# Performance work log

Hardware: AMD Instinct MI355X
Metric: run time of the kernel (lower is better)

## Reference

```python
import jax, jax.numpy as jnp
import numpy as np

N, M, C, IN, OUT = 65536, 512, 512, 256, 256
EPS = 1e-8


def setup_inputs() -> dict:
    key = jax.random.key(0)
    ks = jax.random.split(key, 12)
    d = {}
    d["x"] = jax.random.normal(ks[0], (1, IN), jnp.float32)
    d["memory"] = jax.random.normal(ks[1], (1, N, M), jnp.float32) * 0.05
    d["prev_read"] = jax.random.normal(ks[2], (1, M), jnp.float32) * 0.05
    d["h"] = jnp.ones((1, C), jnp.float32)
    d["c"] = jnp.ones((1, C), jnp.float32)
    d["read_state"] = jnp.zeros((1, N), jnp.float32)
    d["write_state"] = jnp.zeros((1, N), jnp.float32)
    d["W_ih"] = jax.random.normal(ks[3], (4 * C, IN + M), jnp.float32) * 0.02
    d["b_ih"] = jax.random.normal(ks[4], (4 * C,), jnp.float32) * 0.01
    d["W_hh"] = jax.random.normal(ks[5], (4 * C, C), jnp.float32) * 0.02
    d["b_hh"] = jax.random.normal(ks[6], (4 * C,), jnp.float32) * 0.01
    d["W_read"] = jax.random.normal(ks[7], (M + 6, C), jnp.float32) * 0.02
    d["b_read"] = jnp.zeros((M + 6,), jnp.float32)
    d["W_write"] = jax.random.normal(ks[8], (3 * M + 6, C), jnp.float32) * 0.02
    d["b_write"] = jnp.zeros((3 * M + 6,), jnp.float32)
    d["W_out"] = jax.random.normal(ks[9], (OUT, C + M), jnp.float32) * 0.02
    d["b_out"] = jnp.zeros((OUT,), jnp.float32)
    return d


def _address(head_out, w_prev, memory):
    # head_out: [B, M+6(+...)]; returns sharpened addressing weights [B, N]
    key_v = head_out[:, :M]
    beta = jax.nn.softplus(head_out[:, M:M + 1])          # [B,1]
    g = jax.nn.sigmoid(head_out[:, M + 1:M + 2])          # [B,1]
    shift = jax.nn.softmax(head_out[:, M + 2:M + 5], axis=1)  # [B,3]
    gamma = 1.0 + jax.nn.softplus(head_out[:, M + 5:M + 6])   # [B,1]
    # content addressing: cosine similarity over memory rows
    a = memory + EPS                                      # [B,N,M]
    b = key_v[:, None, :] + EPS                           # [B,1,M]
    dot = jnp.sum(a * b, axis=-1)                         # [B,N]
    na = jnp.maximum(jnp.sqrt(jnp.sum(a * a, axis=-1)), EPS)
    nb = jnp.maximum(jnp.sqrt(jnp.sum(b * b, axis=-1)), EPS)
    cos = dot / (na * nb)
    w_context = jax.nn.softmax(beta * cos, axis=1)        # [B,N]
    # NOTE: original code swaps args -> g gates the PREVIOUS weights
    w_interp = g * w_prev + (1.0 - g) * w_context
    # circular shift via 3-tap correlation (conv1d with circular pad)
    w_pad = jnp.concatenate([w_interp[:, -1:], w_interp, w_interp[:, :1]], axis=1)
    w_shift = (w_pad[:, :-2] * shift[:, 0:1]
               + w_pad[:, 1:-1] * shift[:, 1:2]
               + w_pad[:, 2:] * shift[:, 2:3])
    power = w_shift ** gamma
    return power / (jnp.sum(power, axis=1, keepdims=True) + EPS)


def reference(x, memory, prev_read, h, c, read_state, write_state,
              W_ih, b_ih, W_hh, b_hh, W_read, b_read, W_write, b_write,
              W_out, b_out):
    # LSTMCell controller (torch gate order: i, f, g, o)
    inp = jnp.concatenate([x, prev_read], axis=1)                   # [B, IN+M]
    gates = inp @ W_ih.T + b_ih + h @ W_hh.T + b_hh                 # [B, 4C]
    i_g, f_g, g_g, o_g = jnp.split(gates, 4, axis=1)
    c_new = jax.nn.sigmoid(f_g) * c + jax.nn.sigmoid(i_g) * jnp.tanh(g_g)
    h_new = jax.nn.sigmoid(o_g) * jnp.tanh(c_new)

    # read head
    r_out = h_new @ W_read.T + b_read
    w_r = _address(r_out, read_state, memory)                       # [B,N]
    # faithful to torch.matmul([B,N],[B,N,M]).sum(1): sums weights over batch
    read = jnp.einsum('n,bnm->bm', jnp.sum(w_r, axis=0), memory)    # [B,M]

    # write head
    w_out_head = h_new @ W_write.T + b_write
    w_w = _address(w_out_head, write_state, memory)                 # [B,N]
    erase = jax.nn.sigmoid(w_out_head[:, M + 6:2 * M + 6])          # [B,M]
    add = w_out_head[:, 2 * M + 6:3 * M + 6]                        # [B,M]
    memory_new = memory * (1.0 - w_w[:, :, None] * erase[:, None, :]) \
                 + w_w[:, :, None] * add[:, None, :]                # [B,N,M]

    out = jax.nn.sigmoid(jnp.concatenate([h_new, read], axis=1) @ W_out.T + b_out)
    del memory_new  # state update; torch forward returns only the output
    return out
```

## Files before the change

kernel.cpp:

```cpp
#include <hip/hip_runtime.h>
#include <math.h>

#define EPS 1e-8f
#define NN 65536
#define MAGIC 1.0f

#define WS_GATES 0
#define WS_HNEW  2048
#define WS_ROUT  2560
#define WS_PMAX  3104
#define WS_PEXP  5152
#define WS_S     7200
#define WS_PSUM  72736
#define WS_PART  72992
#define WS_FLAGG 204064
#define WS_FLAGP 204192
#define WS_BF    262144

__device__ __forceinline__ float wave_sum(float v) {
    for (int o = 32; o > 0; o >>= 1) v += __shfl_xor(v, o);
    return v;
}
__device__ __forceinline__ float sigm(float x) { return 1.f / (1.f + expf(-x)); }
__device__ __forceinline__ float softplusf_(float x) {
    return x > 20.f ? x : log1pf(expf(x));
}
__device__ __forceinline__ float dot4(float4 a, float4 b) {
    return a.x * b.x + a.y * b.y + a.z * b.z + a.w * b.w;
}
__device__ __forceinline__ float4 ld4(const float* p) { return *(const float4*)p; }

__device__ __forceinline__ float ald(const float* p) {
    return __hip_atomic_load(p, __ATOMIC_RELAXED, __HIP_MEMORY_SCOPE_AGENT);
}
__device__ __forceinline__ float ald_acq(const float* p) {
    return __hip_atomic_load(p, __ATOMIC_ACQUIRE, __HIP_MEMORY_SCOPE_AGENT);
}
__device__ __forceinline__ void ast(float* p, float v) {
    __hip_atomic_store(p, v, __ATOMIC_RELAXED, __HIP_MEMORY_SCOPE_AGENT);
}
__device__ __forceinline__ void ast_rel(float* p, float v) {
    __hip_atomic_store(p, v, __ATOMIC_RELEASE, __HIP_MEMORY_SCOPE_AGENT);
}
__device__ __forceinline__ float2 ald2(const float* p) {
    unsigned long long u = __hip_atomic_load((const unsigned long long*)p,
        __ATOMIC_RELAXED, __HIP_MEMORY_SCOPE_AGENT);
    float2 r; __builtin_memcpy(&r, &u, 8); return r;
}
__device__ __forceinline__ void ast2(float* p, float2 v) {
    unsigned long long u; __builtin_memcpy(&u, &v, 8);
    __hip_atomic_store((unsigned long long*)p, u,
        __ATOMIC_RELAXED, __HIP_MEMORY_SCOPE_AGENT);
}

__device__ __forceinline__ unsigned bf2(float a, float b) {
    unsigned ua = __float_as_uint(a), ub = __float_as_uint(b);
    unsigned ra = (ua + 0x7FFFu + ((ua >> 16) & 1u)) >> 16;
    unsigned rb = (ub + 0x7FFFu + ((ub >> 16) & 1u)) >> 16;
    return ra | (rb << 16);
}

__global__ __launch_bounds__(256) void k_front(const float* __restrict__ x,
                                               const float* __restrict__ pr,
                                               const float* __restrict__ h,
                                               const float* __restrict__ c,
                                               const float* __restrict__ W_ih,
                                               const float* __restrict__ b_ih,
                                               const float* __restrict__ W_hh,
                                               const float* __restrict__ b_hh,
                                               const float* __restrict__ W_read,
                                               const float* __restrict__ b_read,
                                               float* __restrict__ ws) {
    const int b = blockIdx.x, t = threadIdx.x;
    const int lane = t & 63, wv = t >> 6;
    __shared__ float sh[512];

    if (b < 128) {
        #pragma unroll
        for (int i = 0; i < 4; ++i) {
            const int row = b * 16 + wv * 4 + i;
            const float* wi = W_ih + (size_t)row * 768;
            const float* wh = W_hh + (size_t)row * 512;
            float acc = dot4(ld4(wi + lane * 4), ld4(x + lane * 4))
                      + dot4(ld4(wi + 256 + lane * 4), ld4(pr + lane * 4))
                      + dot4(ld4(wi + 512 + lane * 4), ld4(pr + 256 + lane * 4))
                      + dot4(ld4(wh + lane * 4), ld4(h + lane * 4))
                      + dot4(ld4(wh + 256 + lane * 4), ld4(h + 256 + lane * 4));
            acc = wave_sum(acc);
            if (lane == 0) ast(ws + WS_GATES + row, acc + b_ih[row] + b_hh[row]);
        }
        __syncthreads();
        if (t == 0) ast_rel(ws + WS_FLAGG + b, MAGIC);
    }

    if (wv == 0) {
        int cap = 0;
        for (;;) {
            float v0 = ald_acq(ws + WS_FLAGG + lane);
            float v1 = ald_acq(ws + WS_FLAGG + 64 + lane);
            if (__all(v0 == MAGIC && v1 == MAGIC)) break;
            __builtin_amdgcn_s_sleep(1);
            if (++cap > (1 << 20)) break;
        }
    }
    __syncthreads();

    for (int j = t; j < 512; j += 256) {
        float ig = ald(ws + WS_GATES + j);
        float fg = ald(ws + WS_GATES + 512 + j);
        float gg = ald(ws + WS_GATES + 1024 + j);
        float og = ald(ws + WS_GATES + 1536 + j);
        float cn = sigm(fg) * c[j] + sigm(ig) * tanhf(gg);
        float hn = sigm(og) * tanhf(cn);
        sh[j] = hn;
        if (b == 0) ws[WS_HNEW + j] = hn;
    }
    __syncthreads();
    const int o = b * 4 + wv;
    if (o < 518) {
        const float* wr = W_read + (size_t)o * 512;
        float acc = dot4(ld4(wr + lane * 4), ld4(sh + lane * 4))
                  + dot4(ld4(wr + 256 + lane * 4), ld4(sh + 256 + lane * 4));
        acc = wave_sum(acc);
        if (lane == 0) ws[WS_ROUT + o] = acc + b_read[o];
    }
}

__global__ __launch_bounds__(256, 4) void k_cos(const float* __restrict__ mem,
                                                float* __restrict__ ws) {
    const int t = threadIdx.x, lane = t & 63, wv = t >> 6;
    const int gw = blockIdx.x * 4 + wv;
    const float* key = ws + WS_ROUT;
    unsigned short* wsb = (unsigned short*)(ws + WS_BF);
    float4 ka = ld4(key + lane * 4);
    float4 kb = ld4(key + 256 + lane * 4);
    ka.x += EPS; ka.y += EPS; ka.z += EPS; ka.w += EPS;
    kb.x += EPS; kb.y += EPS; kb.z += EPS; kb.w += EPS;
    const float nb = fmaxf(__builtin_amdgcn_sqrtf(
                        wave_sum(dot4(ka, ka) + dot4(kb, kb))), EPS);
    const float beta = softplusf_(key[512]);
    float* sp = ws + WS_S;

    float d[8], q[8];
    #pragma unroll
    for (int grp = 0; grp < 2; ++grp) {
        float4 va[4], vb[4];
        #pragma unroll
        for (int i = 0; i < 4; ++i) {
            const size_t n = (size_t)gw + (grp * 4 + i) * 8192;
            va[i] = ld4(mem + n * 512 + lane * 4);
            vb[i] = ld4(mem + n * 512 + 256 + lane * 4);
        }
        #pragma unroll
        for (int i = 0; i < 4; ++i) {
            const size_t n = (size_t)gw + (grp * 4 + i) * 8192;
            uint2 p0 = make_uint2(bf2(va[i].x, va[i].y), bf2(va[i].z, va[i].w));
            uint2 p1 = make_uint2(bf2(vb[i].x, vb[i].y), bf2(vb[i].z, vb[i].w));
            *(uint2*)(wsb + n * 512 + lane * 4) = p0;
            *(uint2*)(wsb + n * 512 + 256 + lane * 4) = p1;
            va[i].x += EPS; va[i].y += EPS; va[i].z += EPS; va[i].w += EPS;
            vb[i].x += EPS; vb[i].y += EPS; vb[i].z += EPS; vb[i].w += EPS;
            d[grp * 4 + i] = dot4(va[i], ka) + dot4(vb[i], kb);
            q[grp * 4 + i] = dot4(va[i], va[i]) + dot4(vb[i], vb[i]);
        }
    }
    #pragma unroll
    for (int o = 32; o > 0; o >>= 1) {
        #pragma unroll
        for (int i = 0; i < 8; ++i) {
            d[i] += __shfl_xor(d[i], o);
            q[i] += __shfl_xor(q[i], o);
        }
    }
    float sv[8];
    #pragma unroll
    for (int i = 0; i < 8; ++i) {
        float na = fmaxf(__builtin_amdgcn_sqrtf(q[i]), EPS);
        sv[i] = beta * d[i] * __builtin_amdgcn_rcpf(na * nb);
    }
    {
        float mysv = sv[0];
        #pragma unroll
        for (int i = 1; i < 8; ++i) if (lane == i) mysv = sv[i];
        if (lane < 8) sp[gw + lane * 8192] = mysv;
    }
    float m01 = fmaxf(sv[0], sv[1]), m23 = fmaxf(sv[2], sv[3]);
    float m45 = fmaxf(sv[4], sv[5]), m67 = fmaxf(sv[6], sv[7]);
    float m = fmaxf(fmaxf(m01, m23), fmaxf(m45, m67));
    float e = 0.f;
    #pragma unroll
    for (int i = 0; i < 8; ++i) e += __expf(sv[i] - m);

    __shared__ float sm[4], se[4];
    if (lane == 0) { sm[wv] = m; se[wv] = e; }
    __syncthreads();
    if (t == 0) {
        float M = fmaxf(fmaxf(sm[0], sm[1]), fmaxf(sm[2], sm[3]));
        float E = se[0] * __expf(sm[0] - M) + se[1] * __expf(sm[1] - M) +
                  se[2] * __expf(sm[2] - M) + se[3] * __expf(sm[3] - M);
        ws[WS_PMAX + blockIdx.x] = M;
        ws[WS_PEXP + blockIdx.x] = E;
    }
}

__global__ __launch_bounds__(512) void k_readout(const float* __restrict__ rs,
                                                 const float* __restrict__ W_out,
                                                 const float* __restrict__ b_out,
                                                 float* __restrict__ ws,
                                                 float* __restrict__ out) {
    const int b = blockIdx.x, t = threadIdx.x;
    const int lane = t & 63, wv = t >> 6;
    __shared__ float s_m[8], s_e[8];
    __shared__ float wi_l[258];
    __shared__ float pl[256];
    __shared__ float s_ps[4];
    __shared__ float sacc[8][512];
    __shared__ float rd[512];
    __shared__ float s_z[8];

    float m = -1e30f, e = 0.f;
    for (int i = t; i < 2048; i += 512) {
        float bm = ws[WS_PMAX + i], be = ws[WS_PEXP + i];
        float nm = fmaxf(m, bm);
        e = e * expf(m - nm) + be * expf(bm - nm);
        m = nm;
    }
    for (int o = 32; o > 0; o >>= 1) {
        float om = __shfl_xor(m, o), oe = __shfl_xor(e, o);
        float nm = fmaxf(m, om);
        e = e * expf(m - nm) + oe * expf(om - nm);
        m = nm;
    }
    if (lane == 0) { s_m[wv] = m; s_e[wv] = e; }
    __syncthreads();
    float mx = s_m[0];
    for (int i = 1; i < 8; ++i) mx = fmaxf(mx, s_m[i]);
    float Z = 0.f;
    for (int i = 0; i < 8; ++i) Z += s_e[i] * expf(s_m[i] - mx);
    const float invZ = 1.f / Z;
    const float g = sigm(ws[WS_ROUT + 513]);
    float a3 = ws[WS_ROUT + 514], b3 = ws[WS_ROUT + 515], c3 = ws[WS_ROUT + 516];
    float mm = fmaxf(a3, fmaxf(b3, c3));
    float ea = expf(a3 - mm), eb = expf(b3 - mm), ec = expf(c3 - mm);
    float ss = ea + eb + ec;
    const float s0 = ea / ss, s1 = eb / ss, s2 = ec / ss;
    const float gamma = 1.f + softplusf_(ws[WS_ROUT + 517]);

    const int start = b * 256;
    const float* sp = ws + WS_S;
    if (t < 258) {
        int idx = (start - 1 + t) & (NN - 1);
        wi_l[t] = g * rs[idx] + (1.f - g) * expf(sp[idx] - mx) * invZ;
    }
    __syncthreads();
    float ps = 0.f;
    if (t < 256) {
        float wsh = wi_l[t] * s0 + wi_l[t + 1] * s1 + wi_l[t + 2] * s2;
        float pv = powf(wsh, gamma);
        pl[t] = pv;
        ps = pv;
    }
    ps = wave_sum(ps);
    if (t < 256 && lane == 0) s_ps[wv] = ps;
    __syncthreads();
    if (t == 0) ast(ws + WS_PSUM + b, s_ps[0] + s_ps[1] + s_ps[2] + s_ps[3]);

    {
        const unsigned short* wsb = (const unsigned short*)(ws + WS_BF);
        float a0 = 0.f, a1 = 0.f, a2 = 0.f, a3f = 0.f,
              a4 = 0.f, a5 = 0.f, a6 = 0.f, a7 = 0.f;
        #pragma unroll 4
        for (int r = wv; r < 256; r += 8) {
            float w = pl[r];
            uint4 qv = *(const uint4*)(wsb + (size_t)(start + r) * 512 + lane * 8);
            a0 += w * __uint_as_float(qv.x << 16);
            a1 += w * __uint_as_float(qv.x & 0xFFFF0000u);
            a2 += w * __uint_as_float(qv.y << 16);
            a3f += w * __uint_as_float(qv.y & 0xFFFF0000u);
            a4 += w * __uint_as_float(qv.z << 16);
            a5 += w * __uint_as_float(qv.z & 0xFFFF0000u);
            a6 += w * __uint_as_float(qv.w << 16);
            a7 += w * __uint_as_float(qv.w & 0xFFFF0000u);
        }
        float* sw = &sacc[wv][lane * 8];
        sw[0] = a0; sw[1] = a1; sw[2] = a2; sw[3] = a3f;
        sw[4] = a4; sw[5] = a5; sw[6] = a6; sw[7] = a7;
    }
    __syncthreads();
    if (t < 256) {
        const int cc = t * 2;
        float u0 = 0.f, u1 = 0.f;
        #pragma unroll
        for (int w8 = 0; w8 < 8; ++w8) {
            u0 += sacc[w8][cc];
            u1 += sacc[w8][cc + 1];
        }
        ast2(ws + WS_PART + (size_t)b * 512 + cc, make_float2(u0, u1));
    }
    __syncthreads();
    if (t == 0) ast_rel(ws + WS_FLAGP + b, MAGIC);

    if (b >= 32) return;
    if (wv == 0) {
        int cap = 0;
        for (;;) {
            float v0 = ald_acq(ws + WS_FLAGP + lane);
            float v1 = ald_acq(ws + WS_FLAGP + 64 + lane);
            float v2 = ald_acq(ws + WS_FLAGP + 128 + lane);
            float v3 = ald_acq(ws + WS_FLAGP + 192 + lane);
            if (__all(v0 == MAGIC && v1 == MAGIC && v2 == MAGIC && v3 == MAGIC))
                break;
            __builtin_amdgcn_s_sleep(1);
            if (++cap > (1 << 20)) break;
        }
    }
    __syncthreads();
    float z = (t < 256) ? ald(ws + WS_PSUM + t) : 0.f;
    z = wave_sum(z);
    if (lane == 0) s_z[wv] = z;
    __syncthreads();
    float Zp = 0.f;
    for (int i = 0; i < 8; ++i) Zp += s_z[i];
    const float invZp = 1.f / (Zp + EPS);
    if (t < 256) {
        float ax = 0.f, ay = 0.f;
        const float* pp = ws + WS_PART + t * 2;
        #pragma unroll 16
        for (int r = 0; r < 256; ++r) {
            float2 v = ald2(pp + (size_t)r * 512);
            ax += v.x; ay += v.y;
        }
        rd[2 * t] = ax * invZp;
        rd[2 * t + 1] = ay * invZp;
    }
    __syncthreads();
    const int o = b * 8 + wv;
    const float* wo = W_out + (size_t)o * 1024;
    float a = dot4(ld4(wo + lane * 4), ld4(ws + WS_HNEW + lane * 4))
            + dot4(ld4(wo + 256 + lane * 4), ld4(ws + WS_HNEW + 256 + lane * 4))
            + dot4(ld4(wo + 512 + lane * 4), ld4(rd + lane * 4))
            + dot4(ld4(wo + 768 + lane * 4), ld4(rd + 256 + lane * 4));
    a = wave_sum(a);
    if (lane == 0) out[o] = sigm(a + b_out[o]);
}

extern "C" void kernel_launch(void* const* d_in, const int* in_sizes, int n_in,
                              void* d_out, int out_size, void* d_ws, size_t ws_size,
                              hipStream_t stream) {
    const float* x          = (const float*)d_in[0];
    const float* memory     = (const float*)d_in[1];
    const float* prev_read  = (const float*)d_in[2];
    const float* h          = (const float*)d_in[3];
    const float* c          = (const float*)d_in[4];
    const float* read_state = (const float*)d_in[5];
    const float* W_ih   = (const float*)d_in[7];
    const float* b_ih   = (const float*)d_in[8];
    const float* W_hh   = (const float*)d_in[9];
    const float* b_hh   = (const float*)d_in[10];
    const float* W_read = (const float*)d_in[11];
    const float* b_read = (const float*)d_in[12];
    const float* W_out  = (const float*)d_in[15];
    const float* b_out  = (const float*)d_in[16];
    float* ws  = (float*)d_ws;
    float* out = (float*)d_out;

    k_front<<<130, 256, 0, stream>>>(x, prev_read, h, c, W_ih, b_ih, W_hh, b_hh,
                                     W_read, b_read, ws);
    k_cos<<<2048, 256, 0, stream>>>(memory, ws);
    k_readout<<<256, 512, 0, stream>>>(read_state, W_out, b_out, ws, out);
}
```

Before: 77.57 us.

## Split final partial reduction into two levels with extra flag barrier

In the readout kernel, each of the 32 finishing blocks used to reduce all 256 per-block partial vectors on its own. Now each of them first sums 8 partials into a second buffer, signals a new flag, waits for the other 31, and then reduces only 32 vectors. Relaxed atomic loads and stores on the partials become plain accesses ordered by the acquire/release flags. The cosine kernel now issues all eight memory-row loads up front, folds the softmax statistics in online per group of four, and drops its occupancy hint in launch_bounds. The extra grid-wide spin barrier adds latency, and it relies on the new flag area being reset between calls.

```diff
diff --git a/kernel.cpp b/kernel.cpp
--- a/kernel.cpp
+++ b/kernel.cpp
@@ -15,6 +15,8 @@
 #define WS_PART  72992
 #define WS_FLAGG 204064
 #define WS_FLAGP 204192
+#define WS_PART2 204448
+#define WS_FLAG2 220832
 #define WS_BF    262144
 
 __device__ __forceinline__ float wave_sum(float v) {
@@ -41,16 +43,6 @@
 }
 __device__ __forceinline__ void ast_rel(float* p, float v) {
     __hip_atomic_store(p, v, __ATOMIC_RELEASE, __HIP_MEMORY_SCOPE_AGENT);
-}
-__device__ __forceinline__ float2 ald2(const float* p) {
-    unsigned long long u = __hip_atomic_load((const unsigned long long*)p,
-        __ATOMIC_RELAXED, __HIP_MEMORY_SCOPE_AGENT);
-    float2 r; __builtin_memcpy(&r, &u, 8); return r;
-}
-__device__ __forceinline__ void ast2(float* p, float2 v) {
-    unsigned long long u; __builtin_memcpy(&u, &v, 8);
-    __hip_atomic_store((unsigned long long*)p, u,
-        __ATOMIC_RELAXED, __HIP_MEMORY_SCOPE_AGENT);
 }
 
 __device__ __forceinline__ unsigned bf2(float a, float b) {
@@ -126,8 +118,8 @@
     }
 }
 
-__global__ __launch_bounds__(256, 4) void k_cos(const float* __restrict__ mem,
-                                                float* __restrict__ ws) {
+__global__ __launch_bounds__(256) void k_cos(const float* __restrict__ mem,
+                                             float* __restrict__ ws) {
     const int t = threadIdx.x, lane = t & 63, wv = t >> 6;
     const int gw = blockIdx.x * 4 + wv;
     const float* key = ws + WS_ROUT;
@@ -141,55 +133,66 @@
     const float beta = softplusf_(key[512]);
     float* sp = ws + WS_S;
 
-    float d[8], q[8];
+    float4 va[4], vb[4], xa[4], xb[4];
+    #pragma unroll
+    for (int i = 0; i < 4; ++i) {
+        const size_t n = (size_t)gw + i * 8192;
+        va[i] = ld4(mem + n * 512 + lane * 4);
+        vb[i] = ld4(mem + n * 512 + 256 + lane * 4);
+    }
+    #pragma unroll
+    for (int i = 0; i < 4; ++i) {
+        const size_t n = (size_t)gw + (4 + i) * 8192;
+        xa[i] = ld4(mem + n * 512 + lane * 4);
+        xb[i] = ld4(mem + n * 512 + 256 + lane * 4);
+    }
+
+    float m = -1e30f, e = 0.f;
     #pragma unroll
     for (int grp = 0; grp < 2; ++grp) {
-        float4 va[4], vb[4];
+        float d[4], q[4];
         #pragma unroll
         for (int i = 0; i < 4; ++i) {
             const size_t n = (size_t)gw + (grp * 4 + i) * 8192;
-            va[i] = ld4(mem + n * 512 + lane * 4);
-            vb[i] = ld4(mem + n * 512 + 256 + lane * 4);
-        }
+            *(uint2*)(wsb + n * 512 + lane * 4) =
+                make_uint2(bf2(va[i].x, va[i].y), bf2(va[i].z, va[i].w));
+            *(uint2*)(wsb + n * 512 + 256 + lane * 4) =
+                make_uint2(bf2(vb[i].x, vb[i].y), bf2(vb[i].z, vb[i].w));
+            float4 wa = va[i], wb = vb[i];
+            wa.x += EPS; wa.y += EPS; wa.z += EPS; wa.w += EPS;
+            wb.x += EPS; wb.y += EPS; wb.z += EPS; wb.w += EPS;
+            d[i] = dot4(wa, ka) + dot4(wb, kb);
+            q[i] = dot4(wa, wa) + dot4(wb, wb);
+        }
+        if (grp == 0) {
+            #pragma unroll
+            for (int i = 0; i < 4; ++i) { va[i] = xa[i]; vb[i] = xb[i]; }
+        }
+        #pragma unroll
+        for (int o = 32; o > 0; o >>= 1) {
+            #pragma unroll
+            for (int i = 0; i < 4; ++i) {
+                d[i] += __shfl_xor(d[i], o);
+                q[i] += __shfl_xor(q[i], o);
+            }
+        }
+        float sv[4];
         #pragma unroll
         for (int i = 0; i < 4; ++i) {
-            const size_t n = (size_t)gw + (grp * 4 + i) * 8192;
-            uint2 p0 = make_uint2(bf2(va[i].x, va[i].y), bf2(va[i].z, va[i].w));
-            uint2 p1 = make_uint2(bf2(vb[i].x, vb[i].y), bf2(vb[i].z, vb[i].w));
-            *(uint2*)(wsb + n * 512 + lane * 4) = p0;
-            *(uint2*)(wsb + n * 512 + 256 + lane * 4) = p1;
-            va[i].x += EPS; va[i].y += EPS; va[i].z += EPS; va[i].w += EPS;
-            vb[i].x += EPS; vb[i].y += EPS; vb[i].z += EPS; vb[i].w += EPS;
-            d[grp * 4 + i] = dot4(va[i], ka) + dot4(vb[i], kb);
-            q[grp * 4 + i] = dot4(va[i], va[i]) + dot4(vb[i], vb[i]);
-        }
-    }
-    #pragma unroll
-    for (int o = 32; o > 0; o >>= 1) {
-        #pragma unroll
-        for (int i = 0; i < 8; ++i) {
-            d[i] += __shfl_xor(d[i], o);
-            q[i] += __shfl_xor(q[i], o);
-        }
-    }
-    float sv[8];
-    #pragma unroll
-    for (int i = 0; i < 8; ++i) {
-        float na = fmaxf(__builtin_amdgcn_sqrtf(q[i]), EPS);
-        sv[i] = beta * d[i] * __builtin_amdgcn_rcpf(na * nb);
-    }
-    {
+            float na = fmaxf(__builtin_amdgcn_sqrtf(q[i]), EPS);
+            sv[i] = beta * d[i] * __builtin_amdgcn_rcpf(na * nb);
+        }
         float mysv = sv[0];
-        #pragma unroll
-        for (int i = 1; i < 8; ++i) if (lane == i) mysv = sv[i];
-        if (lane < 8) sp[gw + lane * 8192] = mysv;
-    }
-    float m01 = fmaxf(sv[0], sv[1]), m23 = fmaxf(sv[2], sv[3]);
-    float m45 = fmaxf(sv[4], sv[5]), m67 = fmaxf(sv[6], sv[7]);
-    float m = fmaxf(fmaxf(m01, m23), fmaxf(m45, m67));
-    float e = 0.f;
-    #pragma unroll
-    for (int i = 0; i < 8; ++i) e += __expf(sv[i] - m);
+        if (lane == 1) mysv = sv[1];
+        if (lane == 2) mysv = sv[2];
+        if (lane == 3) mysv = sv[3];
+        if (lane < 4) sp[gw + (grp * 4 + lane) * 8192] = mysv;
+        float gm = fmaxf(fmaxf(sv[0], sv[1]), fmaxf(sv[2], sv[3]));
+        float nm = fmaxf(m, gm);
+        e = e * __expf(m - nm) + __expf(sv[0] - nm) + __expf(sv[1] - nm)
+          + __expf(sv[2] - nm) + __expf(sv[3] - nm);
+        m = nm;
+    }
 
     __shared__ float sm[4], se[4];
     if (lane == 0) { sm[wv] = m; se[wv] = e; }
@@ -263,7 +266,7 @@
     ps = wave_sum(ps);
     if (t < 256 && lane == 0) s_ps[wv] = ps;
     __syncthreads();
-    if (t == 0) ast(ws + WS_PSUM + b, s_ps[0] + s_ps[1] + s_ps[2] + s_ps[3]);
+    if (t == 0) ws[WS_PSUM + b] = s_ps[0] + s_ps[1] + s_ps[2] + s_ps[3];
 
     {
         const unsigned short* wsb = (const unsigned short*)(ws + WS_BF);
@@ -295,7 +298,7 @@
             u0 += sacc[w8][cc];
             u1 += sacc[w8][cc + 1];
         }
-        ast2(ws + WS_PART + (size_t)b * 512 + cc, make_float2(u0, u1));
+        *(float2*)(ws + WS_PART + (size_t)b * 512 + cc) = make_float2(u0, u1);
     }
     __syncthreads();
     if (t == 0) ast_rel(ws + WS_FLAGP + b, MAGIC);
@@ -315,7 +318,26 @@
         }
     }
     __syncthreads();
-    float z = (t < 256) ? ald(ws + WS_PSUM + t) : 0.f;
+    {
+        float s = 0.f;
+        #pragma unroll
+        for (int r = 0; r < 8; ++r)
+            s += ws[WS_PART + (size_t)(8 * b + r) * 512 + t];
+        ws[WS_PART2 + (size_t)b * 512 + t] = s;
+    }
+    __syncthreads();
+    if (t == 0) ast_rel(ws + WS_FLAG2 + b, MAGIC);
+    if (wv == 0) {
+        int cap = 0;
+        for (;;) {
+            float v = ald_acq(ws + WS_FLAG2 + (lane & 31));
+            if (__all(v == MAGIC)) break;
+            __builtin_amdgcn_s_sleep(1);
+            if (++cap > (1 << 20)) break;
+        }
+    }
+    __syncthreads();
+    float z = (t < 256) ? ws[WS_PSUM + t] : 0.f;
     z = wave_sum(z);
     if (lane == 0) s_z[wv] = z;
     __syncthreads();
@@ -324,10 +346,9 @@
     const float invZp = 1.f / (Zp + EPS);
     if (t < 256) {
         float ax = 0.f, ay = 0.f;
-        const float* pp = ws + WS_PART + t * 2;
-        #pragma unroll 16
-        for (int r = 0; r < 256; ++r) {
-            float2 v = ald2(pp + (size_t)r * 512);
+        #pragma unroll 8
+        for (int r = 0; r < 32; ++r) {
+            float2 v = *(const float2*)(ws + WS_PART2 + (size_t)r * 512 + t * 2);
             ax += v.x; ay += v.y;
         }
         rd[2 * t] = ax * invZp;
```

Result: faster. 76.01 us (-2.0%).
